# Optimization experiments

Hardware: AMD Instinct MI355X
Metric: run time of the kernel (lower is better)

Reference implementation:

```python
import jax, jax.numpy as jnp
import numpy as np

EPSILON = 0.1
TAU = 1.0
NORM_EPS = 1e-12  # matches torch.nn.functional.normalize eps


def setup_inputs() -> dict:
    key = jax.random.key(0)
    k_ids, k_emb = jax.random.split(key)
    B, T, V, D = 2, 2048, 50257, 768
    input_ids = jax.random.randint(k_ids, (B, T), 0, V, dtype=jnp.int64)
    embedding_weight = jax.random.normal(k_emb, (V, D), dtype=jnp.float32)
    return {"input_ids": input_ids, "embedding_weight": embedding_weight}


def _l2_normalize(x):
    # F.normalize(p=2): x / max(||x||, eps)
    n = jnp.linalg.norm(x, axis=-1, keepdims=True)
    return x / jnp.maximum(n, NORM_EPS)


def reference(input_ids, embedding_weight):
    B, T = input_ids.shape
    V, D = embedding_weight.shape
    # embedding lookup -> (B*T, D)
    vecs = embedding_weight[input_ids].reshape(B * T, D)
    vectors_norm = _l2_normalize(vecs)
    embed_norm = _l2_normalize(embedding_weight)
    # (B*T, V) similarity, scaled by epsilon/2
    scaled_sim = (vectors_norm @ embed_norm.T) * (EPSILON / 2.0)
    # gumbel_softmax (soft, tau=1): softmax((logits + gumbel) / tau)
    gkey = jax.random.key(42)
    gumbel = jax.random.gumbel(gkey, scaled_sim.shape, dtype=scaled_sim.dtype)
    weights = jax.nn.softmax((scaled_sim + gumbel) / TAU, axis=1)
    # mix back through the (unnormalized) embedding table -> (B, T, D)
    selected = weights @ embedding_weight
    return selected.reshape(B, T, D)
```

## Files before the change

### kernel.cpp

```cpp
#include <hip/hip_runtime.h>
#include <stdint.h>

constexpr int VOC  = 50257;
constexpr int VPAD = 50304;
constexpr int DEMB = 768;
constexpr int NQ   = 4096;
constexpr float EPS_HALF = 0.05f;
constexpr float LOG2E = 1.4426950408889634f;
constexpr float C16   = -23.083120654223414f;

typedef __attribute__((ext_vector_type(4))) short    short4_t;
typedef __attribute__((ext_vector_type(8))) short    short8_t;
typedef __attribute__((ext_vector_type(4))) float    float4_t;

__device__ __forceinline__ short f2bf(float f) {
  uint32_t u = __float_as_uint(f);
  u += 0x7FFFu + ((u >> 16) & 1u);
  return (short)(u >> 16);
}
__device__ __forceinline__ float bf2f(short b) {
  return __uint_as_float(((uint32_t)(uint16_t)b) << 16);
}

__device__ __forceinline__ void tf4(uint32_t e0, uint32_t out[4]) {
  const uint32_t K0 = 0u, K1 = 42u, K2 = 0x1BD11BDAu ^ 42u;
  uint32_t x0[4], x1[4];
#pragma unroll
  for (int r = 0; r < 4; ++r) {
    x0[r] = K0;
    x1[r] = (e0 + (uint32_t)r * (uint32_t)VOC) + K1;
  }
#define R4(a) _Pragma("unroll") \
  for (int r = 0; r < 4; ++r) { x0[r] += x1[r]; x1[r] = __builtin_rotateleft32(x1[r], a) ^ x0[r]; }
#define INJ(a, b, i) _Pragma("unroll") \
  for (int r = 0; r < 4; ++r) { x0[r] += (a); x1[r] += (b) + (uint32_t)(i); }
  R4(13) R4(15) R4(26) R4(6)
  INJ(K1, K2, 1)
  R4(17) R4(29) R4(16) R4(24)
  INJ(K2, K0, 2)
  R4(13) R4(15) R4(26) R4(6)
  INJ(K0, K1, 3)
  R4(17) R4(29) R4(16) R4(24)
  INJ(K1, K2, 4)
  R4(13) R4(15) R4(26) R4(6)
#pragma unroll
  for (int r = 0; r < 4; ++r) { x0[r] += K2; x1[r] += K0 + 5u; out[r] = x0[r] ^ x1[r]; }
#undef R4
#undef INJ
}

__device__ __forceinline__ float neg_ln_u(uint32_t bits) {
  uint32_t n = bits >> 9;
  uint32_t m = 8388608u - n;
  float t_log = (23.0f - __builtin_amdgcn_logf((float)n)) * 0.69314718055994531f;
  float x = (float)m * 1.1920928955078125e-7f;
  float t_ser = x * fmaf(x, fmaf(x, fmaf(x, 0.25f, 0.3333333333f), 0.5f), 1.0f);
  return (m < 32768u) ? t_ser : t_log;
}

__global__ void k_prep_e(const float* __restrict__ E, short* __restrict__ Eb,
                         float* __restrict__ rk2) {
  int j = blockIdx.x;
  int t = threadIdx.x;
  __shared__ float red[4];
  float ssq = 0.f;
  if (j < VOC) {
    if (t < 192) {
      float4_t v = *(const float4_t*)(E + (size_t)j * DEMB + t * 4);
      ssq = v[0]*v[0] + v[1]*v[1] + v[2]*v[2] + v[3]*v[3];
      short4_t b; b[0]=f2bf(v[0]); b[1]=f2bf(v[1]); b[2]=f2bf(v[2]); b[3]=f2bf(v[3]);
      *(short4_t*)(Eb + (size_t)j * DEMB + t * 4) = b;
    }
  } else if (t < 192) {
    short4_t z = {0,0,0,0};
    *(short4_t*)(Eb + (size_t)j * DEMB + t * 4) = z;
  }
  for (int off = 32; off; off >>= 1) ssq += __shfl_xor(ssq, off);
  if ((t & 63) == 0) red[t >> 6] = ssq;
  __syncthreads();
  if (t == 0) {
    float s = red[0] + red[1] + red[2] + red[3];
    rk2[j] = (j < VOC) ? (EPS_HALF * LOG2E / fmaxf(sqrtf(s), 1e-12f)) : 0.f;
  }
}

__global__ void k_prep_q(const int* __restrict__ ids, const float* __restrict__ E,
                         short* __restrict__ qn) {
  int p = blockIdx.x;
  int t = threadIdx.x;
  int id = ids[p];
  __shared__ float red[4];
  __shared__ float scale_s;
  float4_t v = {0.f, 0.f, 0.f, 0.f};
  float ssq = 0.f;
  if (t < 192) {
    v = *(const float4_t*)(E + (size_t)id * DEMB + t * 4);
    ssq = v[0]*v[0] + v[1]*v[1] + v[2]*v[2] + v[3]*v[3];
  }
  for (int off = 32; off; off >>= 1) ssq += __shfl_xor(ssq, off);
  if ((t & 63) == 0) red[t >> 6] = ssq;
  __syncthreads();
  if (t == 0) scale_s = 1.0f / fmaxf(sqrtf(red[0]+red[1]+red[2]+red[3]), 1e-12f);
  __syncthreads();
  float sc = scale_s;
  if (t < 192) {
    short4_t b; b[0]=f2bf(v[0]*sc); b[1]=f2bf(v[1]*sc); b[2]=f2bf(v[2]*sc); b[3]=f2bf(v[3]*sc);
    *(short4_t*)(qn + (size_t)p * DEMB + t * 4) = b;
  }
}

__global__ void k_transpose(const short* __restrict__ Eb, short* __restrict__ Et) {
  int lane = threadIdx.x & 63;
  int dg   = threadIdx.x >> 6;
  int key  = blockIdx.x * 64 + lane;
  int d0   = blockIdx.y * 32 + dg * 8;
  short8_t v = *(const short8_t*)(Eb + (size_t)key * DEMB + d0);
#pragma unroll
  for (int q = 0; q < 8; ++q)
    Et[(size_t)(d0 + q) * VPAD + key] = v[q];
}

__global__ void k_zero(float* __restrict__ O, float* __restrict__ lsum) {
  int idx = blockIdx.x * 256 + threadIdx.x;
  if (idx < NQ) lsum[idx] = 0.f;
  float4_t z = {0.f, 0.f, 0.f, 0.f};
  ((float4_t*)O)[idx] = z;
}

__device__ __forceinline__ int swz(int row, int byte) {
  return (row << 7) + (byte ^ ((row & 7) << 4));
}

__device__ __forceinline__ void stage_g2l(short* L, const short* __restrict__ g,
                                          long grow0, long stride, long col0, int tid) {
  int r7 = tid >> 3;
  int c8 = (tid & 7) << 3;
#pragma unroll
  for (int i = 0; i < 4; ++i) {
    int  row = r7 + i * 32;
    long cs  = (long)(c8 ^ ((row & 7) << 3));
    const short* src = g + (grow0 + row) * stride + col0 + cs;
    short* dst = L + row * 64 + c8;
    __builtin_amdgcn_global_load_lds(
        (const __attribute__((address_space(1))) void*)src,
        (__attribute__((address_space(3))) void*)dst, 16, 0, 0);
  }
}

__device__ __forceinline__ short8_t ldfrag(const short* L, int row, int kbyte) {
  return *(const short8_t*)(L + (swz(row, kbyte) >> 1));
}

__global__ __launch_bounds__(256) void k_gemm1(
    const short* __restrict__ qn, const short* __restrict__ Eb,
    const float* __restrict__ rk2, short* __restrict__ P,
    float* __restrict__ lsum, int c0, int KC) {
  __shared__ short lA[128 * 64];
  __shared__ short lB[128 * 64];
  int tid = threadIdx.x, lane = tid & 63;
  int wv = tid >> 6, wr = wv >> 1, wc = wv & 1;
  int rowbase = blockIdx.x * 128;
  int colbase = blockIdx.y * 128;
  float4_t acc[4][4];
  float4_t zero = {0.f, 0.f, 0.f, 0.f};
#pragma unroll
  for (int mt = 0; mt < 4; ++mt)
#pragma unroll
    for (int nt = 0; nt < 4; ++nt) acc[mt][nt] = zero;

  for (int kt = 0; kt < DEMB / 64; ++kt) {
    __syncthreads();
    stage_g2l(lA, qn, rowbase,      DEMB, kt * 64, tid);
    stage_g2l(lB, Eb, c0 + colbase, DEMB, kt * 64, tid);
    __syncthreads();
#pragma unroll
    for (int ks = 0; ks < 2; ++ks) {
      int kb = ks * 64 + (lane >> 4) * 16;
      short8_t a[4], b[4];
#pragma unroll
      for (int mt = 0; mt < 4; ++mt) a[mt] = ldfrag(lA, wr * 64 + mt * 16 + (lane & 15), kb);
#pragma unroll
      for (int nt = 0; nt < 4; ++nt) b[nt] = ldfrag(lB, wc * 64 + nt * 16 + (lane & 15), kb);
#pragma unroll
      for (int mt = 0; mt < 4; ++mt)
#pragma unroll
        for (int nt = 0; nt < 4; ++nt)
          acc[mt][nt] = __builtin_amdgcn_mfma_f32_16x16x32_bf16(a[mt], b[nt], acc[mt][nt], 0, 0, 0);
    }
  }
  int jcb = colbase + wc * 64 + (lane & 15);
  float rkj[4]; bool okj[4];
#pragma unroll
  for (int nt = 0; nt < 4; ++nt) {
    int j = c0 + jcb + nt * 16;
    okj[nt] = j < VOC;
    rkj[nt] = okj[nt] ? rk2[j] : 0.f;
  }
#pragma unroll
  for (int mt = 0; mt < 4; ++mt) {
    int prow = rowbase + wr * 64 + mt * 16 + ((lane >> 4) << 2);
    float rowsum[4] = {0.f, 0.f, 0.f, 0.f};
#pragma unroll
    for (int nt = 0; nt < 4; ++nt) {
      int jc = jcb + nt * 16;
      uint32_t bits[4];
      tf4((uint32_t)prow * (uint32_t)VOC + (uint32_t)(c0 + jc), bits);
#pragma unroll
      for (int r = 0; r < 4; ++r) {
        float t  = neg_ln_u(bits[r]);
        float pe = __builtin_amdgcn_exp2f(fmaf(acc[mt][nt][r], rkj[nt], C16))
                 * __builtin_amdgcn_rcpf(t);
        short pb = okj[nt] ? f2bf(pe) : (short)0;
        rowsum[r] += bf2f(pb);
        P[(size_t)(prow + r) * KC + jc] = pb;
      }
    }
#pragma unroll
    for (int r = 0; r < 4; ++r) {
      float s = rowsum[r];
      s += __shfl_xor(s, 1); s += __shfl_xor(s, 2);
      s += __shfl_xor(s, 4); s += __shfl_xor(s, 8);
      if ((lane & 15) == 0) unsafeAtomicAdd(&lsum[prow + r], s);
    }
  }
}

__global__ __launch_bounds__(256) void k_gemm2(
    const short* __restrict__ P, const short* __restrict__ Et,
    float* __restrict__ O, int c0, int KC, int kseg) {
  __shared__ short lA[128 * 64];
  __shared__ short lB[128 * 64];
  int tid = threadIdx.x, lane = tid & 63;
  int wv = tid >> 6, wr = wv >> 1, wc = wv & 1;
  int rowbase = blockIdx.x * 128;
  int colbase = blockIdx.y * 128;
  int kbase   = blockIdx.z * kseg;
  float4_t acc[4][4];
  float4_t zero = {0.f, 0.f, 0.f, 0.f};
#pragma unroll
  for (int mt = 0; mt < 4; ++mt)
#pragma unroll
    for (int nt = 0; nt < 4; ++nt) acc[mt][nt] = zero;

  for (int kt = 0; kt < kseg / 64; ++kt) {
    __syncthreads();
    stage_g2l(lA, P,  rowbase, KC,   kbase + kt * 64, tid);
    stage_g2l(lB, Et, colbase, VPAD, (long)c0 + kbase + kt * 64, tid);
    __syncthreads();
#pragma unroll
    for (int ks = 0; ks < 2; ++ks) {
      int kb = ks * 64 + (lane >> 4) * 16;
      short8_t a[4], b[4];
#pragma unroll
      for (int mt = 0; mt < 4; ++mt) a[mt] = ldfrag(lA, wr * 64 + mt * 16 + (lane & 15), kb);
#pragma unroll
      for (int nt = 0; nt < 4; ++nt) b[nt] = ldfrag(lB, wc * 64 + nt * 16 + (lane & 15), kb);
#pragma unroll
      for (int mt = 0; mt < 4; ++mt)
#pragma unroll
        for (int nt = 0; nt < 4; ++nt)
          acc[mt][nt] = __builtin_amdgcn_mfma_f32_16x16x32_bf16(a[mt], b[nt], acc[mt][nt], 0, 0, 0);
    }
  }
#pragma unroll
  for (int mt = 0; mt < 4; ++mt)
#pragma unroll
    for (int nt = 0; nt < 4; ++nt) {
      int d = colbase + wc * 64 + nt * 16 + (lane & 15);
#pragma unroll
      for (int r = 0; r < 4; ++r) {
        int p = rowbase + wr * 64 + mt * 16 + ((lane >> 4) << 2) + r;
        unsafeAtomicAdd(&O[(size_t)p * DEMB + d], acc[mt][nt][r]);
      }
    }
}

__global__ void k_finalize(const float* __restrict__ O, const float* __restrict__ lsum,
                           float* __restrict__ out) {
  int idx = blockIdx.x * 256 + threadIdx.x;
  float inv = 1.0f / lsum[idx / 192];
  float4_t v = ((const float4_t*)O)[idx];
  v[0]*=inv; v[1]*=inv; v[2]*=inv; v[3]*=inv;
  ((float4_t*)out)[idx] = v;
}

extern "C" void kernel_launch(void* const* d_in, const int* in_sizes, int n_in,
                              void* d_out, int out_size, void* d_ws, size_t ws_size,
                              hipStream_t stream) {
  (void)in_sizes; (void)n_in; (void)out_size;
  const int*   ids = (const int*)d_in[0];
  const float* E   = (const float*)d_in[1];
  float*       out = (float*)d_out;

  char* w = (char*)d_ws;
  short* Eb = (short*)w;      w += (size_t)VPAD * DEMB * 2;
  short* Et = (short*)w;      w += (size_t)DEMB * VPAD * 2;
  short* qn = (short*)w;      w += (size_t)NQ * DEMB * 2;
  float* O  = (float*)w;      w += (size_t)NQ * DEMB * 4;
  float* rk2 = (float*)w;     w += (size_t)VPAD * 4;
  float* lsum = (float*)w;    w += NQ * 4;
  short* P  = (short*)w;
  size_t fixed = (size_t)(w - (char*)d_ws);

  int KC = 2048;
  if      (fixed + (size_t)NQ * 8192 * 2 <= ws_size) KC = 8192;
  else if (fixed + (size_t)NQ * 4096 * 2 <= ws_size) KC = 4096;
  int chunks = (VPAD + KC - 1) / KC;

  k_zero<<<(NQ * DEMB / 4) / 256, 256, 0, stream>>>(O, lsum);
  k_prep_e<<<VPAD, 256, 0, stream>>>(E, Eb, rk2);
  k_prep_q<<<NQ, 256, 0, stream>>>(ids, E, qn);
  k_transpose<<<dim3(VPAD / 64, DEMB / 32), 256, 0, stream>>>(Eb, Et);

  for (int c = 0; c < chunks; ++c) {
    int c0 = c * KC;
    int KCeff = VPAD - c0; if (KCeff > KC) KCeff = KC;
    k_gemm1<<<dim3(NQ / 128, KCeff / 128), 256, 0, stream>>>(qn, Eb, rk2, P, lsum, c0, KC);
    int KS = 4;
    while (KS > 1 && (KCeff % (KS * 64)) != 0) KS >>= 1;
    k_gemm2<<<dim3(NQ / 128, DEMB / 128, KS), 256, 0, stream>>>(P, Et, O, c0, KC, KCeff / KS);
  }
  k_finalize<<<(NQ * DEMB / 4) / 256, 256, 0, stream>>>(O, lsum, out);
}
```

Baseline: 1.560 ms.

## Split Gumbel softmax epilogue out of GEMM1 into separate vectorized kernel

GEMM1 now writes the raw similarity as fp16 into the chunk buffer. A new k_gumbel kernel then rereads it row-contiguously, runs the Threefry hash for 8 consecutive columns per thread, applies the exp and gumbel scaling, and writes packed bf16 probabilities in place. It also does a wave-level row-sum reduction with fewer atomics. This takes the scattered per-element stores and heavy RNG register pressure out of the MFMA kernel, but it adds an extra read and write pass over the P buffer and an extra launch per chunk. Storing the similarity in fp16 adds rounding before the exponent.

```diff
diff --git a/kernel.cpp b/kernel.cpp
--- a/kernel.cpp
+++ b/kernel.cpp
@@ -12,41 +12,36 @@
 typedef __attribute__((ext_vector_type(4))) short    short4_t;
 typedef __attribute__((ext_vector_type(8))) short    short8_t;
 typedef __attribute__((ext_vector_type(4))) float    float4_t;
+typedef __attribute__((ext_vector_type(4))) uint32_t uint4_t;
 
 __device__ __forceinline__ short f2bf(float f) {
   uint32_t u = __float_as_uint(f);
   u += 0x7FFFu + ((u >> 16) & 1u);
   return (short)(u >> 16);
 }
-__device__ __forceinline__ float bf2f(short b) {
-  return __uint_as_float(((uint32_t)(uint16_t)b) << 16);
-}
-
-__device__ __forceinline__ void tf4(uint32_t e0, uint32_t out[4]) {
+
+__device__ __forceinline__ void tf8(uint32_t e0, uint32_t out[8]) {
   const uint32_t K0 = 0u, K1 = 42u, K2 = 0x1BD11BDAu ^ 42u;
-  uint32_t x0[4], x1[4];
-#pragma unroll
-  for (int r = 0; r < 4; ++r) {
-    x0[r] = K0;
-    x1[r] = (e0 + (uint32_t)r * (uint32_t)VOC) + K1;
-  }
-#define R4(a) _Pragma("unroll") \
-  for (int r = 0; r < 4; ++r) { x0[r] += x1[r]; x1[r] = __builtin_rotateleft32(x1[r], a) ^ x0[r]; }
-#define INJ(a, b, i) _Pragma("unroll") \
-  for (int r = 0; r < 4; ++r) { x0[r] += (a); x1[r] += (b) + (uint32_t)(i); }
-  R4(13) R4(15) R4(26) R4(6)
-  INJ(K1, K2, 1)
-  R4(17) R4(29) R4(16) R4(24)
-  INJ(K2, K0, 2)
-  R4(13) R4(15) R4(26) R4(6)
-  INJ(K0, K1, 3)
-  R4(17) R4(29) R4(16) R4(24)
-  INJ(K1, K2, 4)
-  R4(13) R4(15) R4(26) R4(6)
-#pragma unroll
-  for (int r = 0; r < 4; ++r) { x0[r] += K2; x1[r] += K0 + 5u; out[r] = x0[r] ^ x1[r]; }
-#undef R4
-#undef INJ
+  uint32_t x0[8], x1[8];
+#pragma unroll
+  for (int r = 0; r < 8; ++r) { x0[r] = K0; x1[r] = e0 + (uint32_t)r + K1; }
+#define R8(a) _Pragma("unroll") \
+  for (int r = 0; r < 8; ++r) { x0[r] += x1[r]; x1[r] = __builtin_rotateleft32(x1[r], a) ^ x0[r]; }
+#define INJ8(a, b, i) _Pragma("unroll") \
+  for (int r = 0; r < 8; ++r) { x0[r] += (a); x1[r] += (b) + (uint32_t)(i); }
+  R8(13) R8(15) R8(26) R8(6)
+  INJ8(K1, K2, 1)
+  R8(17) R8(29) R8(16) R8(24)
+  INJ8(K2, K0, 2)
+  R8(13) R8(15) R8(26) R8(6)
+  INJ8(K0, K1, 3)
+  R8(17) R8(29) R8(16) R8(24)
+  INJ8(K1, K2, 4)
+  R8(13) R8(15) R8(26) R8(6)
+#pragma unroll
+  for (int r = 0; r < 8; ++r) { x0[r] += K2; x1[r] += K0 + 5u; out[r] = x0[r] ^ x1[r]; }
+#undef R8
+#undef INJ8
 }
 
 __device__ __forceinline__ float neg_ln_u(uint32_t bits) {
@@ -153,8 +148,7 @@
 
 __global__ __launch_bounds__(256) void k_gemm1(
     const short* __restrict__ qn, const short* __restrict__ Eb,
-    const float* __restrict__ rk2, short* __restrict__ P,
-    float* __restrict__ lsum, int c0, int KC) {
+    _Float16* __restrict__ S, int c0, int KC) {
   __shared__ short lA[128 * 64];
   __shared__ short lB[128 * 64];
   int tid = threadIdx.x, lane = tid & 63;
@@ -188,41 +182,59 @@
           acc[mt][nt] = __builtin_amdgcn_mfma_f32_16x16x32_bf16(a[mt], b[nt], acc[mt][nt], 0, 0, 0);
     }
   }
-  int jcb = colbase + wc * 64 + (lane & 15);
-  float rkj[4]; bool okj[4];
-#pragma unroll
-  for (int nt = 0; nt < 4; ++nt) {
-    int j = c0 + jcb + nt * 16;
-    okj[nt] = j < VOC;
-    rkj[nt] = okj[nt] ? rk2[j] : 0.f;
-  }
 #pragma unroll
   for (int mt = 0; mt < 4; ++mt) {
     int prow = rowbase + wr * 64 + mt * 16 + ((lane >> 4) << 2);
-    float rowsum[4] = {0.f, 0.f, 0.f, 0.f};
-#pragma unroll
-    for (int nt = 0; nt < 4; ++nt) {
-      int jc = jcb + nt * 16;
-      uint32_t bits[4];
-      tf4((uint32_t)prow * (uint32_t)VOC + (uint32_t)(c0 + jc), bits);
-#pragma unroll
-      for (int r = 0; r < 4; ++r) {
-        float t  = neg_ln_u(bits[r]);
-        float pe = __builtin_amdgcn_exp2f(fmaf(acc[mt][nt][r], rkj[nt], C16))
-                 * __builtin_amdgcn_rcpf(t);
-        short pb = okj[nt] ? f2bf(pe) : (short)0;
-        rowsum[r] += bf2f(pb);
-        P[(size_t)(prow + r) * KC + jc] = pb;
-      }
-    }
+    int jc0  = colbase + wc * 64 + (lane & 15);
 #pragma unroll
     for (int r = 0; r < 4; ++r) {
-      float s = rowsum[r];
-      s += __shfl_xor(s, 1); s += __shfl_xor(s, 2);
-      s += __shfl_xor(s, 4); s += __shfl_xor(s, 8);
-      if ((lane & 15) == 0) unsafeAtomicAdd(&lsum[prow + r], s);
-    }
-  }
+      _Float16* dst = S + (size_t)(prow + r) * KC + jc0;
+#pragma unroll
+      for (int nt = 0; nt < 4; ++nt) dst[nt * 16] = (_Float16)acc[mt][nt][r];
+    }
+  }
+}
+
+__global__ __launch_bounds__(256) void k_gumbel(
+    uint32_t* __restrict__ SP, const float* __restrict__ rk2,
+    float* __restrict__ lsum, int c0, int KCeff, int KC) {
+  int p    = blockIdx.x;
+  int colq = blockIdx.y * 2048 + threadIdx.x * 8;
+  float partial = 0.f;
+  if (colq < KCeff) {
+    uint32_t* base = SP + ((size_t)p * KC + colq) / 2;
+    uint4_t sv = *(const uint4_t*)base;
+    int j0 = c0 + colq;
+    float4_t rk_lo = *(const float4_t*)(rk2 + j0);
+    float4_t rk_hi = *(const float4_t*)(rk2 + j0 + 4);
+    uint32_t bits[8];
+    tf8((uint32_t)p * (uint32_t)VOC + (uint32_t)j0, bits);
+    float pe[8];
+#pragma unroll
+    for (int i = 0; i < 8; ++i) {
+      uint32_t h = (sv[i >> 1] >> ((i & 1) * 16)) & 0xFFFFu;
+      float sim = (float)__uint_as_float((h << 16) >> 16 | 0u) * 0.f;
+      (void)sim;
+      _Float16 hf = *(_Float16*)&h;
+      float simf = (float)hf;
+      float rkj = (i < 4) ? rk_lo[i] : rk_hi[i - 4];
+      float t = neg_ln_u(bits[i]);
+      float v = __builtin_amdgcn_exp2f(fmaf(simf, rkj, C16)) * __builtin_amdgcn_rcpf(t);
+      bool ok = (j0 + i) < VOC;
+      pe[i] = ok ? v : 0.f;
+      partial += pe[i];
+    }
+    uint4_t pkv;
+#pragma unroll
+    for (int i = 0; i < 4; ++i) {
+      uint32_t r;
+      asm("v_cvt_pk_bf16_f32 %0, %1, %2" : "=v"(r) : "v"(pe[2 * i]), "v"(pe[2 * i + 1]));
+      pkv[i] = r;
+    }
+    *(uint4_t*)base = pkv;
+  }
+  for (int off = 32; off; off >>= 1) partial += __shfl_xor(partial, off);
+  if ((threadIdx.x & 63) == 0 && partial != 0.f) unsafeAtomicAdd(&lsum[p], partial);
 }
 
 __global__ __launch_bounds__(256) void k_gemm2(
@@ -299,7 +311,7 @@
   float* O  = (float*)w;      w += (size_t)NQ * DEMB * 4;
   float* rk2 = (float*)w;     w += (size_t)VPAD * 4;
   float* lsum = (float*)w;    w += NQ * 4;
-  short* P  = (short*)w;
+  void*  SP = (void*)w;
   size_t fixed = (size_t)(w - (char*)d_ws);
 
   int KC = 2048;
@@ -315,10 +327,13 @@
   for (int c = 0; c < chunks; ++c) {
     int c0 = c * KC;
     int KCeff = VPAD - c0; if (KCeff > KC) KCeff = KC;
-    k_gemm1<<<dim3(NQ / 128, KCeff / 128), 256, 0, stream>>>(qn, Eb, rk2, P, lsum, c0, KC);
+    k_gemm1<<<dim3(NQ / 128, KCeff / 128), 256, 0, stream>>>(qn, Eb, (_Float16*)SP, c0, KC);
+    k_gumbel<<<dim3(NQ, (KCeff + 2047) / 2048), 256, 0, stream>>>(
+        (uint32_t*)SP, rk2, lsum, c0, KCeff, KC);
     int KS = 4;
     while (KS > 1 && (KCeff % (KS * 64)) != 0) KS >>= 1;
-    k_gemm2<<<dim3(NQ / 128, DEMB / 128, KS), 256, 0, stream>>>(P, Et, O, c0, KC, KCeff / KS);
+    k_gemm2<<<dim3(NQ / 128, DEMB / 128, KS), 256, 0, stream>>>(
+        (const short*)SP, Et, O, c0, KC, KCeff / KS);
   }
   k_finalize<<<(NQ * DEMB / 4) / 256, 256, 0, stream>>>(O, lsum, out);
 }
```

Measured after the change: 1.621 ms. 3.9% more time.
